# Performance work log

Measured on AMD Instinct MI355X. Metric: run time of the kernel, lower is better.

## Reference

```python
import jax, jax.numpy as jnp
import numpy as np

H = 128          # num_hidden
NIN = 256        # num_in (2*H: edge feat + gathered node feat)
B, L, K = 2, 2048, 48
SCALE = 30.0
LN_EPS = 1e-5


def _layer_norm(x, g, b):
    mu = jnp.mean(x, axis=-1, keepdims=True)
    var = jnp.var(x, axis=-1, keepdims=True)
    return g * (x - mu) * jax.lax.rsqrt(var + LN_EPS) + b


def _gather_nodes(nodes, idx):
    # nodes: [B,L,C], idx: [B,L,K] -> [B,L,K,C]
    return jax.vmap(lambda n, i: n[i])(nodes, idx)


def _gelu(x):
    return jax.nn.gelu(x, approximate=False)  # torch GELU default (erf)


def setup_inputs() -> dict:
    key = jax.random.key(0)
    ks = jax.random.split(key, 24)
    p = lambda k, shp: (jax.random.normal(k, shp, jnp.float32) * 0.05)
    inp = {
        "h_V": jax.random.normal(ks[0], (B, L, H), jnp.float32),
        "h_E": jax.random.normal(ks[1], (B, L, K, H), jnp.float32),
        "E_idx": jax.random.randint(ks[2], (B, L, K), 0, L),
        "mask_V": jnp.ones((B, L), jnp.float32),
        "mask_attend": jnp.ones((B, L, K), jnp.float32),
        # node-message MLP W1-W2-W3
        "W1": p(ks[3], (H + NIN, H)), "b1": jnp.zeros((H,), jnp.float32),
        "W2": p(ks[4], (H, H)), "b2": jnp.zeros((H,), jnp.float32),
        "W3": p(ks[5], (H, H)), "b3": jnp.zeros((H,), jnp.float32),
        # edge-update MLP W11-W12-W13
        "W11": p(ks[6], (H + NIN, H)), "b11": jnp.zeros((H,), jnp.float32),
        "W12": p(ks[7], (H, H)), "b12": jnp.zeros((H,), jnp.float32),
        "W13": p(ks[8], (H, H)), "b13": jnp.zeros((H,), jnp.float32),
        # layer norms
        "g1": jnp.ones((H,), jnp.float32), "be1": jnp.zeros((H,), jnp.float32),
        "g2": jnp.ones((H,), jnp.float32), "be2": jnp.zeros((H,), jnp.float32),
        "g3": jnp.ones((H,), jnp.float32), "be3": jnp.zeros((H,), jnp.float32),
        # position-wise FFN (H -> 4H -> H)
        "W_in": p(ks[9], (H, 4 * H)), "b_in": jnp.zeros((4 * H,), jnp.float32),
        "W_out": p(ks[10], (4 * H, H)), "b_out": jnp.zeros((H,), jnp.float32),
    }
    return inp


def reference(h_V, h_E, E_idx, mask_V, mask_attend,
              W1, b1, W2, b2, W3, b3,
              W11, b11, W12, b12, W13, b13,
              g1, be1, g2, be2, g3, be3,
              W_in, b_in, W_out, b_out):
    # ---- node update: gather neighbors, concat, 3-layer MLP, masked sum ----
    h_nb = _gather_nodes(h_V, E_idx)                       # [B,L,K,H]
    h_EV = jnp.concatenate(
        [jnp.broadcast_to(h_V[:, :, None, :], h_nb.shape), h_E, h_nb], axis=-1)
    h_msg = _gelu(h_EV @ W1 + b1)
    h_msg = _gelu(h_msg @ W2 + b2)
    h_msg = h_msg @ W3 + b3                                # [B,L,K,H]
    h_msg = mask_attend[..., None] * h_msg
    dh = jnp.sum(h_msg, axis=-2) / SCALE                   # [B,L,H]
    h_V = _layer_norm(h_V + dh, g1, be1)
    # ---- position-wise FFN + residual ----
    dh = _gelu(h_V @ W_in + b_in) @ W_out + b_out
    h_V = _layer_norm(h_V + dh, g2, be2)
    h_V = mask_V[..., None] * h_V
    # ---- edge update ----
    h_nb = _gather_nodes(h_V, E_idx)
    h_EV = jnp.concatenate(
        [jnp.broadcast_to(h_V[:, :, None, :], h_nb.shape), h_E, h_nb], axis=-1)
    h_msg = _gelu(h_EV @ W11 + b11)
    h_msg = _gelu(h_msg @ W12 + b12)
    h_msg = h_msg @ W13 + b13
    h_E = _layer_norm(h_E + h_msg, g3, be3)
    return h_V, h_E
```

## Files before the change

### kernel.cpp

```cpp
#include <hip/hip_runtime.h>
#include <hip/hip_bf16.h>
#include <math.h>

#define Hdim 128
#define Kn 48
#define NN 4096
#define FFH 512
#define LN_EPS 1e-5f

typedef __attribute__((ext_vector_type(8))) short bf16x8;
typedef __attribute__((ext_vector_type(4))) float floatx4;
typedef unsigned short ushort_t;

__device__ __forceinline__ float gelu_f(float x) {
    float x2 = x * x;
    float u = x * fmaf(x2, -0.1029454f, -2.3022081f);
    return x * __builtin_amdgcn_rcpf(1.0f + exp2f(u));
}

__device__ __forceinline__ ushort_t f2bf(float f) {
    union { float f; unsigned u; } v;
    v.f = f;
    unsigned r = v.u + 0x7FFF + ((v.u >> 16) & 1);
    return (ushort_t)(r >> 16);
}
__device__ __forceinline__ float bf2f(ushort_t h) {
    union { unsigned u; float f; } v;
    v.u = ((unsigned)h) << 16;
    return v.f;
}

__global__ __launch_bounds__(256) void convert_all(
    const float* __restrict__ W1, const float* __restrict__ W11,
    const float* __restrict__ W2, const float* __restrict__ W3,
    const float* __restrict__ W12, const float* __restrict__ W13,
    const float* __restrict__ W_in, const float* __restrict__ W_out,
    const float* __restrict__ hV, ushort_t* __restrict__ Wt1m,
    ushort_t* __restrict__ Wt11m, ushort_t* __restrict__ Wt2,
    ushort_t* __restrict__ Wt3, ushort_t* __restrict__ Wt12,
    ushort_t* __restrict__ Wt13, ushort_t* __restrict__ WtIn,
    ushort_t* __restrict__ WtOut, ushort_t* __restrict__ hVbf) {
    const int b = blockIdx.x, t = threadIdx.x;
    if (b < 128) {
        int s = b * 256 + t, k = s >> 7, n = s & 127;
        Wt1m[n * 256 + k] = f2bf(W1[16384 + s]);
    } else if (b < 256) {
        int s = (b - 128) * 256 + t, k = s >> 7, n = s & 127;
        Wt11m[n * 256 + k] = f2bf(W11[16384 + s]);
    } else if (b < 320) {
        int s = (b - 256) * 256 + t, k = s >> 7, n = s & 127;
        Wt2[n * 128 + k] = f2bf(W2[s]);
    } else if (b < 384) {
        int s = (b - 320) * 256 + t, k = s >> 7, n = s & 127;
        Wt3[n * 128 + k] = f2bf(W3[s]);
    } else if (b < 448) {
        int s = (b - 384) * 256 + t, k = s >> 7, n = s & 127;
        Wt12[n * 128 + k] = f2bf(W12[s]);
    } else if (b < 512) {
        int s = (b - 448) * 256 + t, k = s >> 7, n = s & 127;
        Wt13[n * 128 + k] = f2bf(W13[s]);
    } else if (b < 768) {
        int s = (b - 512) * 256 + t, k = s >> 9, n = s & 511;
        WtIn[n * 128 + k] = f2bf(W_in[s]);
    } else if (b < 1024) {
        int s = (b - 768) * 256 + t, k = s >> 7, n = s & 127;
        WtOut[n * 512 + k] = f2bf(W_out[s]);
    } else {
        int i = (b - 1024) * 256 + t;
        float4 a = *(const float4*)(hV + (size_t)i * 8);
        float4 c = *(const float4*)(hV + (size_t)i * 8 + 4);
        ushort_t o[8] = {f2bf(a.x), f2bf(a.y), f2bf(a.z), f2bf(a.w),
                         f2bf(c.x), f2bf(c.y), f2bf(c.z), f2bf(c.w)};
        *(uint4*)(hVbf + (size_t)i * 8) = *(const uint4*)o;
    }
}

__global__ __launch_bounds__(128) void pre_self(const float* __restrict__ hV,
                                                const float* __restrict__ W,
                                                const float* __restrict__ b,
                                                float* __restrict__ selfA) {
    __shared__ __align__(16) float xs[8][Hdim];
    const int o = threadIdx.x;
    const int n0 = blockIdx.x * 8;
    for (int n = 0; n < 8; ++n) xs[n][o] = hV[(size_t)(n0 + n) * Hdim + o];
    __syncthreads();
    float acc[8];
    const float bo = b[o];
#pragma unroll
    for (int n = 0; n < 8; ++n) acc[n] = bo;
    for (int i = 0; i < Hdim; i += 4) {
        const float w0 = W[(i + 0) * Hdim + o];
        const float w1 = W[(i + 1) * Hdim + o];
        const float w2 = W[(i + 2) * Hdim + o];
        const float w3 = W[(i + 3) * Hdim + o];
#pragma unroll
        for (int n = 0; n < 8; ++n) {
            const float4 v = *(const float4*)&xs[n][i];
            acc[n] = fmaf(v.x, w0, acc[n]);
            acc[n] = fmaf(v.y, w1, acc[n]);
            acc[n] = fmaf(v.z, w2, acc[n]);
            acc[n] = fmaf(v.w, w3, acc[n]);
        }
    }
#pragma unroll
    for (int n = 0; n < 8; ++n) selfA[(size_t)(n0 + n) * Hdim + o] = acc[n];
}

template <int MODE>
__global__ __launch_bounds__(256, 3) void edge_mlp(
    const float* __restrict__ hV, const float* __restrict__ hE,
    const int* __restrict__ Eidx, const float* __restrict__ maskAtt,
    const float* __restrict__ selfA, const ushort_t* __restrict__ hVbf,
    const ushort_t* __restrict__ WtA, const ushort_t* __restrict__ WtB,
    const ushort_t* __restrict__ WtC, const float* __restrict__ bias2,
    const float* __restrict__ bias3, const float* __restrict__ gamma,
    const float* __restrict__ beta, float* __restrict__ outp) {
    __shared__ __align__(16) char T0[24576];
    __shared__ __align__(16) char T1[12288];
    __shared__ __align__(16) char T2[12288];
    __shared__ int idx_s[Kn];
    __shared__ float dh_s[128];
    __shared__ float rsum[Kn][4], rsum2[Kn][4];
    __shared__ float mu_s[Kn], rs_s[Kn];
    __shared__ float rw[8];

    const int tid = threadIdx.x;
    const int lane = tid & 63;
    const int w = tid >> 6;
    const int l15 = lane & 15, l4 = lane >> 4;
    const int n = blockIdx.x;
    const int n0 = w * 32;
    const int bbase = (n >> 11) << 11;

    if (tid < Kn) idx_s[tid] = Eidx[(size_t)n * Kn + tid];
    {
        const float4* src = (const float4*)(hE + (size_t)n * Kn * Hdim);
#pragma unroll
        for (int it = 0; it < 6; ++it) {
            int i = tid + it * 256;
            float4 v = src[i];
            int row = i >> 5, c = i & 31;
            unsigned lo = f2bf(v.x) | ((unsigned)f2bf(v.y) << 16);
            unsigned hi = f2bf(v.z) | ((unsigned)f2bf(v.w) << 16);
            *(uint2*)(T0 + row * 512 + ((c * 8) ^ ((row & 7) << 4))) =
                make_uint2(lo, hi);
        }
    }
    __syncthreads();
#pragma unroll
    for (int it = 0; it < 3; ++it) {
        int i = tid + it * 256;
        int row = i >> 4, c = i & 15;
        uint4 v =
            *(const uint4*)(hVbf + (size_t)(bbase + idx_s[row]) * Hdim + c * 8);
        *(uint4*)(T0 + row * 512 + ((256 + c * 16) ^ ((row & 7) << 4))) = v;
    }
    __syncthreads();

    floatx4 acc[3][2];
#pragma unroll
    for (int mt = 0; mt < 3; ++mt)
#pragma unroll
        for (int nt = 0; nt < 2; ++nt) acc[mt][nt] = (floatx4)0.0f;

#pragma unroll
    for (int kk = 0; kk < 8; ++kk) {
        bf16x8 a[3], bb[2];
#pragma unroll
        for (int mt = 0; mt < 3; ++mt) {
            int row = mt * 16 + l15;
            a[mt] = *(const bf16x8*)(T0 + row * 512 +
                     ((kk * 64 + l4 * 16) ^ ((row & 7) << 4)));
        }
#pragma unroll
        for (int nt = 0; nt < 2; ++nt)
            bb[nt] = *(const bf16x8*)(WtA + (n0 + nt * 16 + l15) * 256 +
                                      kk * 32 + l4 * 8);
#pragma unroll
        for (int mt = 0; mt < 3; ++mt)
#pragma unroll
            for (int nt = 0; nt < 2; ++nt)
                acc[mt][nt] = __builtin_amdgcn_mfma_f32_16x16x32_bf16(
                    a[mt], bb[nt], acc[mt][nt], 0, 0, 0);
    }
    {
        float sA[2];
#pragma unroll
        for (int nt = 0; nt < 2; ++nt)
            sA[nt] = selfA[(size_t)n * Hdim + n0 + nt * 16 + l15];
#pragma unroll
        for (int mt = 0; mt < 3; ++mt)
#pragma unroll
            for (int nt = 0; nt < 2; ++nt) {
                const int col = n0 + nt * 16 + l15;
#pragma unroll
                for (int r = 0; r < 4; ++r) {
                    float v = gelu_f(acc[mt][nt][r] + sA[nt]);
                    int row = mt * 16 + l4 * 4 + r;
                    *(ushort_t*)(T1 + row * 256 +
                                 ((col * 2) ^ ((row & 7) << 4))) = f2bf(v);
                }
            }
    }
    __syncthreads();

    {
        float bv[2];
#pragma unroll
        for (int nt = 0; nt < 2; ++nt) bv[nt] = bias2[n0 + nt * 16 + l15];
#pragma unroll
        for (int mt = 0; mt < 3; ++mt)
#pragma unroll
            for (int nt = 0; nt < 2; ++nt)
                acc[mt][nt] = (floatx4){bv[nt], bv[nt], bv[nt], bv[nt]};
    }
#pragma unroll
    for (int kk = 0; kk < 4; ++kk) {
        bf16x8 a[3], bb[2];
#pragma unroll
        for (int mt = 0; mt < 3; ++mt) {
            int row = mt * 16 + l15;
            a[mt] = *(const bf16x8*)(T1 + row * 256 +
                     ((kk * 64 + l4 * 16) ^ ((row & 7) << 4)));
        }
#pragma unroll
        for (int nt = 0; nt < 2; ++nt)
            bb[nt] = *(const bf16x8*)(WtB + (n0 + nt * 16 + l15) * 128 +
                                      kk * 32 + l4 * 8);
#pragma unroll
        for (int mt = 0; mt < 3; ++mt)
#pragma unroll
            for (int nt = 0; nt < 2; ++nt)
                acc[mt][nt] = __builtin_amdgcn_mfma_f32_16x16x32_bf16(
                    a[mt], bb[nt], acc[mt][nt], 0, 0, 0);
    }
#pragma unroll
    for (int mt = 0; mt < 3; ++mt)
#pragma unroll
        for (int nt = 0; nt < 2; ++nt) {
            const int col = n0 + nt * 16 + l15;
#pragma unroll
            for (int r = 0; r < 4; ++r) {
                float v = gelu_f(acc[mt][nt][r]);
                int row = mt * 16 + l4 * 4 + r;
                *(ushort_t*)(T2 + row * 256 + ((col * 2) ^ ((row & 7) << 4))) =
                    f2bf(v);
            }
        }
    __syncthreads();

    {
        float bv[2];
#pragma unroll
        for (int nt = 0; nt < 2; ++nt) bv[nt] = bias3[n0 + nt * 16 + l15];
#pragma unroll
        for (int mt = 0; mt < 3; ++mt)
#pragma unroll
            for (int nt = 0; nt < 2; ++nt)
                acc[mt][nt] = (floatx4){bv[nt], bv[nt], bv[nt], bv[nt]};
    }
#pragma unroll
    for (int kk = 0; kk < 4; ++kk) {
        bf16x8 a[3], bb[2];
#pragma unroll
        for (int mt = 0; mt < 3; ++mt) {
            int row = mt * 16 + l15;
            a[mt] = *(const bf16x8*)(T2 + row * 256 +
                     ((kk * 64 + l4 * 16) ^ ((row & 7) << 4)));
        }
#pragma unroll
        for (int nt = 0; nt < 2; ++nt)
            bb[nt] = *(const bf16x8*)(WtC + (n0 + nt * 16 + l15) * 128 +
                                      kk * 32 + l4 * 8);
#pragma unroll
        for (int mt = 0; mt < 3; ++mt)
#pragma unroll
            for (int nt = 0; nt < 2; ++nt)
                acc[mt][nt] = __builtin_amdgcn_mfma_f32_16x16x32_bf16(
                    a[mt], bb[nt], acc[mt][nt], 0, 0, 0);
    }

    if (MODE == 0) {
        float mav[3][4];
#pragma unroll
        for (int mt = 0; mt < 3; ++mt)
#pragma unroll
            for (int r = 0; r < 4; ++r)
                mav[mt][r] =
                    maskAtt[(size_t)n * Kn + mt * 16 + l4 * 4 + r];
#pragma unroll
        for (int nt = 0; nt < 2; ++nt) {
            float c = 0.0f;
#pragma unroll
            for (int mt = 0; mt < 3; ++mt)
#pragma unroll
                for (int r = 0; r < 4; ++r)
                    c = fmaf(mav[mt][r], acc[mt][nt][r], c);
            c += __shfl_xor(c, 16);
            c += __shfl_xor(c, 32);
            if (l4 == 0) dh_s[n0 + nt * 16 + l15] = c;
        }
        __syncthreads();
        float x = 0.0f;
        if (tid < 128) {
            x = hV[(size_t)n * Hdim + tid] + dh_s[tid] * (1.0f / 30.0f);
            float s = x, s2 = x * x;
#pragma unroll
            for (int off = 32; off > 0; off >>= 1) {
                s += __shfl_xor(s, off);
                s2 += __shfl_xor(s2, off);
            }
            if (lane == 0) {
                rw[(tid >> 6) * 2] = s;
                rw[(tid >> 6) * 2 + 1] = s2;
            }
        }
        __syncthreads();
        if (tid < 128) {
            const float ts = rw[0] + rw[2], ts2 = rw[1] + rw[3];
            const float mu = ts * (1.0f / Hdim);
            const float var = ts2 * (1.0f / Hdim) - mu * mu;
            const float rs = rsqrtf(var + LN_EPS);
            outp[(size_t)n * Hdim + tid] =
                gamma[tid] * (x - mu) * rs + beta[tid];
        }
    } else {
        float xv[3][2][4];
#pragma unroll
        for (int mt = 0; mt < 3; ++mt)
#pragma unroll
            for (int nt = 0; nt < 2; ++nt) {
                const int col = n0 + nt * 16 + l15;
#pragma unroll
                for (int r = 0; r < 4; ++r) {
                    int row = mt * 16 + l4 * 4 + r;
                    ushort_t hv = *(const ushort_t*)(
                        T0 + row * 512 + ((col * 2) ^ ((row & 7) << 4)));
                    xv[mt][nt][r] = acc[mt][nt][r] + bf2f(hv);
                }
            }
#pragma unroll
        for (int mt = 0; mt < 3; ++mt)
#pragma unroll
            for (int r = 0; r < 4; ++r) {
                float s = xv[mt][0][r] + xv[mt][1][r];
                float s2 = xv[mt][0][r] * xv[mt][0][r] +
                           xv[mt][1][r] * xv[mt][1][r];
#pragma unroll
                for (int off = 1; off < 16; off <<= 1) {
                    s += __shfl_xor(s, off);
                    s2 += __shfl_xor(s2, off);
                }
                if (l15 == 0) {
                    int row = mt * 16 + l4 * 4 + r;
                    rsum[row][w] = s;
                    rsum2[row][w] = s2;
                }
            }
        __syncthreads();
        if (tid < Kn) {
            float s = rsum[tid][0] + rsum[tid][1] + rsum[tid][2] + rsum[tid][3];
            float s2 =
                rsum2[tid][0] + rsum2[tid][1] + rsum2[tid][2] + rsum2[tid][3];
            float mu = s * (1.0f / Hdim);
            float var = s2 * (1.0f / Hdim) - mu * mu;
            mu_s[tid] = mu;
            rs_s[tid] = rsqrtf(var + LN_EPS);
        }
        __syncthreads();
        float gv[2], bv[2];
#pragma unroll
        for (int nt = 0; nt < 2; ++nt) {
            gv[nt] = gamma[n0 + nt * 16 + l15];
            bv[nt] = beta[n0 + nt * 16 + l15];
        }
#pragma unroll
        for (int mt = 0; mt < 3; ++mt)
#pragma unroll
            for (int nt = 0; nt < 2; ++nt) {
                const int col = n0 + nt * 16 + l15;
#pragma unroll
                for (int r = 0; r < 4; ++r) {
                    int row = mt * 16 + l4 * 4 + r;
                    float y = gv[nt] * (xv[mt][nt][r] - mu_s[row]) *
                                  rs_s[row] + bv[nt];
                    outp[((size_t)n * Kn + row) * Hdim + col] = y;
                }
            }
    }
}

__global__ __launch_bounds__(512) void ffn_mfma(
    const float* __restrict__ hV2, const ushort_t* __restrict__ WtIn,
    const float* __restrict__ b_in, const ushort_t* __restrict__ WtOut,
    const float* __restrict__ b_out, const float* __restrict__ g2,
    const float* __restrict__ be2, const float* __restrict__ maskV,
    float* __restrict__ outp, ushort_t* __restrict__ outb) {
    __shared__ __align__(16) char XF[8192];
    __shared__ __align__(16) char HF[32768];
    __shared__ float rsF[32][4], rs2F[32][4], muF[32], rstdF[32];

    const int tid = threadIdx.x;
    const int lane = tid & 63;
    const int w = tid >> 6;
    const int wm = w >> 2, wc = w & 3;
    const int l15 = lane & 15, l4 = lane >> 4;
    const int rg0 = blockIdx.x * 32;

    {
        const float4* src = (const float4*)(hV2 + (size_t)rg0 * Hdim);
#pragma unroll
        for (int it = 0; it < 2; ++it) {
            int i = tid + it * 512;
            float4 v = src[i];
            int row = i >> 5, c = i & 31;
            unsigned lo = f2bf(v.x) | ((unsigned)f2bf(v.y) << 16);
            unsigned hi = f2bf(v.z) | ((unsigned)f2bf(v.w) << 16);
            *(uint2*)(XF + row * 256 + ((c * 8) ^ ((row & 7) << 4))) =
                make_uint2(lo, hi);
        }
    }
    __syncthreads();
    {
        floatx4 a1[8];
#pragma unroll
        for (int j = 0; j < 8; ++j) {
            float bv = b_in[wc * 128 + j * 16 + l15];
            a1[j] = (floatx4){bv, bv, bv, bv};
        }
#pragma unroll
        for (int kk = 0; kk < 4; ++kk) {
            int row = wm * 16 + l15;
            bf16x8 af = *(const bf16x8*)(XF + row * 256 +
                         ((kk * 64 + l4 * 16) ^ ((row & 7) << 4)));
#pragma unroll
            for (int j = 0; j < 8; ++j) {
                bf16x8 bf = *(const bf16x8*)(WtIn +
                             (wc * 128 + j * 16 + l15) * 128 + kk * 32 +
                             l4 * 8);
                a1[j] = __builtin_amdgcn_mfma_f32_16x16x32_bf16(af, bf, a1[j],
                                                                0, 0, 0);
            }
        }
#pragma unroll
        for (int j = 0; j < 8; ++j) {
            const int col = wc * 128 + j * 16 + l15;
#pragma unroll
            for (int r = 0; r < 4; ++r) {
                int row = wm * 16 + l4 * 4 + r;
                float v = gelu_f(a1[j][r]);
                *(ushort_t*)(HF + row * 1024 +
                             ((col * 2) ^ ((row & 7) << 4))) = f2bf(v);
            }
        }
    }
    __syncthreads();
    floatx4 o2[2];
#pragma unroll
    for (int nt = 0; nt < 2; ++nt) {
        float bv = b_out[(wc * 2 + nt) * 16 + l15];
        o2[nt] = (floatx4){bv, bv, bv, bv};
    }
#pragma unroll
    for (int kk = 0; kk < 16; ++kk) {
        int row = wm * 16 + l15;
        bf16x8 af = *(const bf16x8*)(HF + row * 1024 +
                     ((kk * 64 + l4 * 16) ^ ((row & 7) << 4)));
#pragma unroll
        for (int nt = 0; nt < 2; ++nt) {
            bf16x8 bf = *(const bf16x8*)(WtOut +
                         ((wc * 2 + nt) * 16 + l15) * 512 + kk * 32 + l4 * 8);
            o2[nt] = __builtin_amdgcn_mfma_f32_16x16x32_bf16(af, bf, o2[nt],
                                                             0, 0, 0);
        }
    }
    float xv[2][4];
#pragma unroll
    for (int nt = 0; nt < 2; ++nt) {
        const int col = (wc * 2 + nt) * 16 + l15;
#pragma unroll
        for (int r = 0; r < 4; ++r) {
            int row = wm * 16 + l4 * 4 + r;
            xv[nt][r] = hV2[(size_t)(rg0 + row) * Hdim + col] + o2[nt][r];
        }
    }
#pragma unroll
    for (int r = 0; r < 4; ++r) {
        float s = xv[0][r] + xv[1][r];
        float s2 = xv[0][r] * xv[0][r] + xv[1][r] * xv[1][r];
#pragma unroll
        for (int off = 1; off < 16; off <<= 1) {
            s += __shfl_xor(s, off);
            s2 += __shfl_xor(s2, off);
        }
        if (l15 == 0) {
            int row = wm * 16 + l4 * 4 + r;
            rsF[row][wc] = s;
            rs2F[row][wc] = s2;
        }
    }
    __syncthreads();
    if (tid < 32) {
        float s = rsF[tid][0] + rsF[tid][1] + rsF[tid][2] + rsF[tid][3];
        float s2 = rs2F[tid][0] + rs2F[tid][1] + rs2F[tid][2] + rs2F[tid][3];
        float mu = s * (1.0f / Hdim);
        float var = s2 * (1.0f / Hdim) - mu * mu;
        muF[tid] = mu;
        rstdF[tid] = rsqrtf(var + LN_EPS);
    }
    __syncthreads();
#pragma unroll
    for (int nt = 0; nt < 2; ++nt) {
        const int col = (wc * 2 + nt) * 16 + l15;
        float gvv = g2[col], bvv = be2[col];
#pragma unroll
        for (int r = 0; r < 4; ++r) {
            int row = wm * 16 + l4 * 4 + r;
            float y = (gvv * (xv[nt][r] - muF[row]) * rstdF[row] + bvv) *
                      maskV[rg0 + row];
            outp[(size_t)(rg0 + row) * Hdim + col] = y;
            outb[(size_t)(rg0 + row) * Hdim + col] = f2bf(y);
        }
    }
}

extern "C" void kernel_launch(void* const* d_in, const int* in_sizes, int n_in,
                              void* d_out, int out_size, void* d_ws,
                              size_t ws_size, hipStream_t stream) {
    const float* hV = (const float*)d_in[0];
    const float* hE = (const float*)d_in[1];
    const int* Eidx = (const int*)d_in[2];
    const float* maskV = (const float*)d_in[3];
    const float* maskAtt = (const float*)d_in[4];
    const float* W1 = (const float*)d_in[5];
    const float* b1 = (const float*)d_in[6];
    const float* W2 = (const float*)d_in[7];
    const float* b2 = (const float*)d_in[8];
    const float* W3 = (const float*)d_in[9];
    const float* b3 = (const float*)d_in[10];
    const float* W11 = (const float*)d_in[11];
    const float* b11 = (const float*)d_in[12];
    const float* W12 = (const float*)d_in[13];
    const float* b12 = (const float*)d_in[14];
    const float* W13 = (const float*)d_in[15];
    const float* b13 = (const float*)d_in[16];
    const float* g1 = (const float*)d_in[17];
    const float* be1 = (const float*)d_in[18];
    const float* g2 = (const float*)d_in[19];
    const float* be2 = (const float*)d_in[20];
    const float* g3 = (const float*)d_in[21];
    const float* be3 = (const float*)d_in[22];
    const float* W_in = (const float*)d_in[23];
    const float* b_in = (const float*)d_in[24];
    const float* W_out = (const float*)d_in[25];
    const float* b_out = (const float*)d_in[26];

    float* out_hV = (float*)d_out;
    float* out_hE = out_hV + (size_t)NN * Hdim;
    float* ws = (float*)d_ws;
    float* hV2 = ws;
    float* selfA = ws + 524288;
    ushort_t* u = (ushort_t*)(ws + 1048576);
    ushort_t* hVbf = u;
    ushort_t* outVbf = u + 524288;
    ushort_t* Wt1m = u + 1048576;
    ushort_t* Wt11m = u + 1081344;
    ushort_t* Wt2 = u + 1114112;
    ushort_t* Wt3 = u + 1130496;
    ushort_t* Wt12 = u + 1146880;
    ushort_t* Wt13 = u + 1163264;
    ushort_t* WtIn = u + 1179648;
    ushort_t* WtOut = u + 1245184;

    convert_all<<<1280, 256, 0, stream>>>(W1, W11, W2, W3, W12, W13, W_in,
                                          W_out, hV, Wt1m, Wt11m, Wt2, Wt3,
                                          Wt12, Wt13, WtIn, WtOut, hVbf);
    pre_self<<<NN / 8, 128, 0, stream>>>(hV, W1, b1, selfA);
    edge_mlp<0><<<NN, 256, 0, stream>>>(hV, hE, Eidx, maskAtt, selfA, hVbf,
                                        Wt1m, Wt2, Wt3, b2, b3, g1, be1, hV2);
    ffn_mfma<<<NN / 32, 512, 0, stream>>>(hV2, WtIn, b_in, WtOut, b_out, g2,
                                          be2, maskV, out_hV, outVbf);
    pre_self<<<NN / 8, 128, 0, stream>>>(out_hV, W11, b11, selfA);
    edge_mlp<1><<<NN, 256, 0, stream>>>(nullptr, hE, Eidx, nullptr, selfA,
                                        outVbf, Wt11m, Wt12, Wt13, b12, b13,
                                        g3, be3, out_hE);
}
```

Baseline: 411.5 us.

## Fuse self-projection into convert and FFN kernels, pre-tile weights for MFMA

Removes the two standalone pre_self launches. The first self-projection moves into convert_all, and the second into the FFN kernel, which now does a bf16 MFMA against a new W11 self-part weight. Weights are pre-packed into an MFMA fragment-tiled layout through a shared-memory transpose. Edge and FFN shared tiles switch to a column-major padded layout. T2 now aliases T0, which cuts shared memory so edge_mlp can request 4 blocks per SM, at the cost of an extra barrier. The FFN is retiled to 16 rows per block, and the second self-projection now runs in bf16, which slightly changes precision.

```diff
diff --git a/kernel.cpp b/kernel.cpp
--- a/kernel.cpp
+++ b/kernel.cpp
@@ -12,6 +12,8 @@
 typedef __attribute__((ext_vector_type(4))) float floatx4;
 typedef unsigned short ushort_t;
 
+#define CMA(row, col) ((((col) >> 3) * 784) + ((row) << 4) + (((col)&7) << 1))
+
 __device__ __forceinline__ float gelu_f(float x) {
     float x2 = x * x;
     float u = x * fmaf(x2, -0.1029454f, -2.3022081f);
@@ -19,10 +21,8 @@
 }
 
 __device__ __forceinline__ ushort_t f2bf(float f) {
-    union { float f; unsigned u; } v;
-    v.f = f;
-    unsigned r = v.u + 0x7FFF + ((v.u >> 16) & 1);
-    return (ushort_t)(r >> 16);
+    __hip_bfloat16 h = __float2bfloat16(f);
+    return *reinterpret_cast<ushort_t*>(&h);
 }
 __device__ __forceinline__ float bf2f(ushort_t h) {
     union { unsigned u; float f; } v;
@@ -35,79 +35,91 @@
     const float* __restrict__ W2, const float* __restrict__ W3,
     const float* __restrict__ W12, const float* __restrict__ W13,
     const float* __restrict__ W_in, const float* __restrict__ W_out,
-    const float* __restrict__ hV, ushort_t* __restrict__ Wt1m,
-    ushort_t* __restrict__ Wt11m, ushort_t* __restrict__ Wt2,
+    const float* __restrict__ hV, const float* __restrict__ b1,
+    ushort_t* __restrict__ Wt1m, ushort_t* __restrict__ Wt11m,
+    ushort_t* __restrict__ Wt11a, ushort_t* __restrict__ Wt2,
     ushort_t* __restrict__ Wt3, ushort_t* __restrict__ Wt12,
     ushort_t* __restrict__ Wt13, ushort_t* __restrict__ WtIn,
-    ushort_t* __restrict__ WtOut, ushort_t* __restrict__ hVbf) {
+    ushort_t* __restrict__ WtOut, ushort_t* __restrict__ hVbf,
+    float* __restrict__ selfA) {
+    __shared__ __align__(16) char cmem[8448];
     const int b = blockIdx.x, t = threadIdx.x;
-    if (b < 128) {
-        int s = b * 256 + t, k = s >> 7, n = s & 127;
-        Wt1m[n * 256 + k] = f2bf(W1[16384 + s]);
-    } else if (b < 256) {
-        int s = (b - 128) * 256 + t, k = s >> 7, n = s & 127;
-        Wt11m[n * 256 + k] = f2bf(W11[16384 + s]);
-    } else if (b < 320) {
-        int s = (b - 256) * 256 + t, k = s >> 7, n = s & 127;
-        Wt2[n * 128 + k] = f2bf(W2[s]);
-    } else if (b < 384) {
-        int s = (b - 320) * 256 + t, k = s >> 7, n = s & 127;
-        Wt3[n * 128 + k] = f2bf(W3[s]);
-    } else if (b < 448) {
-        int s = (b - 384) * 256 + t, k = s >> 7, n = s & 127;
-        Wt12[n * 128 + k] = f2bf(W12[s]);
-    } else if (b < 512) {
-        int s = (b - 448) * 256 + t, k = s >> 7, n = s & 127;
-        Wt13[n * 128 + k] = f2bf(W13[s]);
-    } else if (b < 768) {
-        int s = (b - 512) * 256 + t, k = s >> 9, n = s & 511;
-        WtIn[n * 128 + k] = f2bf(W_in[s]);
-    } else if (b < 1024) {
-        int s = (b - 768) * 256 + t, k = s >> 7, n = s & 127;
-        WtOut[n * 512 + k] = f2bf(W_out[s]);
-    } else {
-        int i = (b - 1024) * 256 + t;
-        float4 a = *(const float4*)(hV + (size_t)i * 8);
-        float4 c = *(const float4*)(hV + (size_t)i * 8 + 4);
+
+    if (b < 272) {
+        const float* src;
+        ushort_t* dst;
+        int K, C, rowOff, tile;
+        if (b < 32)       { src = W1;   dst = Wt1m;  K = 256; C = 128; rowOff = 128; tile = b; }
+        else if (b < 64)  { src = W11;  dst = Wt11m; K = 256; C = 128; rowOff = 128; tile = b - 32; }
+        else if (b < 80)  { src = W11;  dst = Wt11a; K = 128; C = 128; rowOff = 0;   tile = b - 64; }
+        else if (b < 96)  { src = W2;   dst = Wt2;   K = 128; C = 128; rowOff = 0;   tile = b - 80; }
+        else if (b < 112) { src = W3;   dst = Wt3;   K = 128; C = 128; rowOff = 0;   tile = b - 96; }
+        else if (b < 128) { src = W12;  dst = Wt12;  K = 128; C = 128; rowOff = 0;   tile = b - 112; }
+        else if (b < 144) { src = W13;  dst = Wt13;  K = 128; C = 128; rowOff = 0;   tile = b - 128; }
+        else if (b < 208) { src = W_in; dst = WtIn;  K = 128; C = 512; rowOff = 0;   tile = b - 144; }
+        else              { src = W_out;dst = WtOut; K = 512; C = 128; rowOff = 0;   tile = b - 208; }
+        const int tpr = C >> 5;
+        const int tk = tile / tpr, tn = tile % tpr;
+        const int tr0 = tk * 32, tc0 = tn * 32;
+        const int KD32 = K >> 5;
+        float (*s)[33] = (float(*)[33])cmem;
+#pragma unroll
+        for (int i = 0; i < 4; ++i) {
+            int r = (t >> 5) + i * 8, c = t & 31;
+            s[r][c] = src[(size_t)(rowOff + tr0 + r) * C + tc0 + c];
+        }
+        __syncthreads();
+        if (t < 128) {
+            int n_loc = t >> 2, kc0 = (t & 3) * 8;
+            int n = tc0 + n_loc, k = tr0 + kc0;
+            ushort_t o[8];
+#pragma unroll
+            for (int e = 0; e < 8; ++e) o[e] = f2bf(s[kc0 + e][n_loc]);
+            size_t idx = (size_t)((n >> 4) * KD32 + (k >> 5)) * 512 +
+                         ((k >> 3) & 3) * 128 + (n & 15) * 8;
+            *(uint4*)(dst + idx) = *(const uint4*)o;
+        }
+    } else if (b < 528) {
+        int i = (b - 272) * 2048 + t * 8;
+        float4 a = *(const float4*)(hV + (size_t)i);
+        float4 c = *(const float4*)(hV + (size_t)i + 4);
         ushort_t o[8] = {f2bf(a.x), f2bf(a.y), f2bf(a.z), f2bf(a.w),
                          f2bf(c.x), f2bf(c.y), f2bf(c.z), f2bf(c.w)};
-        *(uint4*)(hVbf + (size_t)i * 8) = *(const uint4*)o;
-    }
-}
-
-__global__ __launch_bounds__(128) void pre_self(const float* __restrict__ hV,
-                                                const float* __restrict__ W,
-                                                const float* __restrict__ b,
-                                                float* __restrict__ selfA) {
-    __shared__ __align__(16) float xs[8][Hdim];
-    const int o = threadIdx.x;
-    const int n0 = blockIdx.x * 8;
-    for (int n = 0; n < 8; ++n) xs[n][o] = hV[(size_t)(n0 + n) * Hdim + o];
-    __syncthreads();
-    float acc[8];
-    const float bo = b[o];
-#pragma unroll
-    for (int n = 0; n < 8; ++n) acc[n] = bo;
-    for (int i = 0; i < Hdim; i += 4) {
-        const float w0 = W[(i + 0) * Hdim + o];
-        const float w1 = W[(i + 1) * Hdim + o];
-        const float w2 = W[(i + 2) * Hdim + o];
-        const float w3 = W[(i + 3) * Hdim + o];
-#pragma unroll
-        for (int n = 0; n < 8; ++n) {
-            const float4 v = *(const float4*)&xs[n][i];
-            acc[n] = fmaf(v.x, w0, acc[n]);
-            acc[n] = fmaf(v.y, w1, acc[n]);
-            acc[n] = fmaf(v.z, w2, acc[n]);
-            acc[n] = fmaf(v.w, w3, acc[n]);
-        }
-    }
-#pragma unroll
-    for (int n = 0; n < 8; ++n) selfA[(size_t)(n0 + n) * Hdim + o] = acc[n];
+        *(uint4*)(hVbf + (size_t)i) = *(const uint4*)o;
+    } else {
+        float (*xs)[Hdim] = (float(*)[Hdim])cmem;
+        const int grp = t >> 7, o = t & 127;
+        const int nb0 = (b - 528) * 16;
+#pragma unroll
+        for (int n = 0; n < 8; ++n)
+            xs[grp * 8 + n][o] = hV[(size_t)(nb0 + grp * 8 + n) * Hdim + o];
+        __syncthreads();
+        float acc[8];
+        const float bo = b1[o];
+#pragma unroll
+        for (int n = 0; n < 8; ++n) acc[n] = bo;
+        for (int i = 0; i < Hdim; i += 4) {
+            const float w0 = W1[(i + 0) * Hdim + o];
+            const float w1 = W1[(i + 1) * Hdim + o];
+            const float w2 = W1[(i + 2) * Hdim + o];
+            const float w3 = W1[(i + 3) * Hdim + o];
+#pragma unroll
+            for (int n = 0; n < 8; ++n) {
+                const float4 v = *(const float4*)&xs[grp * 8 + n][i];
+                acc[n] = fmaf(v.x, w0, acc[n]);
+                acc[n] = fmaf(v.y, w1, acc[n]);
+                acc[n] = fmaf(v.z, w2, acc[n]);
+                acc[n] = fmaf(v.w, w3, acc[n]);
+            }
+        }
+#pragma unroll
+        for (int n = 0; n < 8; ++n)
+            selfA[(size_t)(nb0 + grp * 8 + n) * Hdim + o] = acc[n];
+    }
 }
 
 template <int MODE>
-__global__ __launch_bounds__(256, 3) void edge_mlp(
+__global__ __launch_bounds__(256, 4) void edge_mlp(
     const float* __restrict__ hV, const float* __restrict__ hE,
     const int* __restrict__ Eidx, const float* __restrict__ maskAtt,
     const float* __restrict__ selfA, const ushort_t* __restrict__ hVbf,
@@ -115,14 +127,14 @@
     const ushort_t* __restrict__ WtC, const float* __restrict__ bias2,
     const float* __restrict__ bias3, const float* __restrict__ gamma,
     const float* __restrict__ beta, float* __restrict__ outp) {
-    __shared__ __align__(16) char T0[24576];
-    __shared__ __align__(16) char T1[12288];
-    __shared__ __align__(16) char T2[12288];
+    __shared__ __align__(16) char T0[32 * 784];
+    __shared__ __align__(16) char T1[16 * 784];
     __shared__ int idx_s[Kn];
     __shared__ float dh_s[128];
     __shared__ float rsum[Kn][4], rsum2[Kn][4];
     __shared__ float mu_s[Kn], rs_s[Kn];
     __shared__ float rw[8];
+    char* T2 = T0 + 16 * 784;
 
     const int tid = threadIdx.x;
     const int lane = tid & 63;
@@ -131,6 +143,8 @@
     const int n = blockIdx.x;
     const int n0 = w * 32;
     const int bbase = (n >> 11) << 11;
+    const int abase = l4 * 784 + l15 * 16;
+    const int fbase = l4 * 128 + l15 * 8;
 
     if (tid < Kn) idx_s[tid] = Eidx[(size_t)n * Kn + tid];
     {
@@ -139,10 +153,10 @@
         for (int it = 0; it < 6; ++it) {
             int i = tid + it * 256;
             float4 v = src[i];
-            int row = i >> 5, c = i & 31;
+            int row = i >> 5, j = i & 31;
             unsigned lo = f2bf(v.x) | ((unsigned)f2bf(v.y) << 16);
             unsigned hi = f2bf(v.z) | ((unsigned)f2bf(v.w) << 16);
-            *(uint2*)(T0 + row * 512 + ((c * 8) ^ ((row & 7) << 4))) =
+            *(uint2*)(T0 + (j >> 1) * 784 + row * 16 + (j & 1) * 8) =
                 make_uint2(lo, hi);
         }
     }
@@ -153,7 +167,7 @@
         int row = i >> 4, c = i & 15;
         uint4 v =
             *(const uint4*)(hVbf + (size_t)(bbase + idx_s[row]) * Hdim + c * 8);
-        *(uint4*)(T0 + row * 512 + ((256 + c * 16) ^ ((row & 7) << 4))) = v;
+        *(uint4*)(T0 + (16 + c) * 784 + row * 16) = v;
     }
     __syncthreads();
 
@@ -167,15 +181,12 @@
     for (int kk = 0; kk < 8; ++kk) {
         bf16x8 a[3], bb[2];
 #pragma unroll
-        for (int mt = 0; mt < 3; ++mt) {
-            int row = mt * 16 + l15;
-            a[mt] = *(const bf16x8*)(T0 + row * 512 +
-                     ((kk * 64 + l4 * 16) ^ ((row & 7) << 4)));
-        }
+        for (int mt = 0; mt < 3; ++mt)
+            a[mt] = *(const bf16x8*)(T0 + abase + mt * 256 + kk * 3136);
 #pragma unroll
         for (int nt = 0; nt < 2; ++nt)
-            bb[nt] = *(const bf16x8*)(WtA + (n0 + nt * 16 + l15) * 256 +
-                                      kk * 32 + l4 * 8);
+            bb[nt] = *(const bf16x8*)(WtA + ((w * 2 + nt) * 8 + kk) * 512 +
+                                      fbase);
 #pragma unroll
         for (int mt = 0; mt < 3; ++mt)
 #pragma unroll
@@ -197,8 +208,7 @@
                 for (int r = 0; r < 4; ++r) {
                     float v = gelu_f(acc[mt][nt][r] + sA[nt]);
                     int row = mt * 16 + l4 * 4 + r;
-                    *(ushort_t*)(T1 + row * 256 +
-                                 ((col * 2) ^ ((row & 7) << 4))) = f2bf(v);
+                    *(ushort_t*)(T1 + CMA(row, col)) = f2bf(v);
                 }
             }
     }
@@ -218,15 +228,12 @@
     for (int kk = 0; kk < 4; ++kk) {
         bf16x8 a[3], bb[2];
 #pragma unroll
-        for (int mt = 0; mt < 3; ++mt) {
-            int row = mt * 16 + l15;
-            a[mt] = *(const bf16x8*)(T1 + row * 256 +
-                     ((kk * 64 + l4 * 16) ^ ((row & 7) << 4)));
-        }
+        for (int mt = 0; mt < 3; ++mt)
+            a[mt] = *(const bf16x8*)(T1 + abase + mt * 256 + kk * 3136);
 #pragma unroll
         for (int nt = 0; nt < 2; ++nt)
-            bb[nt] = *(const bf16x8*)(WtB + (n0 + nt * 16 + l15) * 128 +
-                                      kk * 32 + l4 * 8);
+            bb[nt] = *(const bf16x8*)(WtB + ((w * 2 + nt) * 4 + kk) * 512 +
+                                      fbase);
 #pragma unroll
         for (int mt = 0; mt < 3; ++mt)
 #pragma unroll
@@ -234,6 +241,7 @@
                 acc[mt][nt] = __builtin_amdgcn_mfma_f32_16x16x32_bf16(
                     a[mt], bb[nt], acc[mt][nt], 0, 0, 0);
     }
+    __syncthreads();
 #pragma unroll
     for (int mt = 0; mt < 3; ++mt)
 #pragma unroll
@@ -243,8 +251,7 @@
             for (int r = 0; r < 4; ++r) {
                 float v = gelu_f(acc[mt][nt][r]);
                 int row = mt * 16 + l4 * 4 + r;
-                *(ushort_t*)(T2 + row * 256 + ((col * 2) ^ ((row & 7) << 4))) =
-                    f2bf(v);
+                *(ushort_t*)(T2 + CMA(row, col)) = f2bf(v);
             }
         }
     __syncthreads();
@@ -263,15 +270,12 @@
     for (int kk = 0; kk < 4; ++kk) {
         bf16x8 a[3], bb[2];
 #pragma unroll
-        for (int mt = 0; mt < 3; ++mt) {
-            int row = mt * 16 + l15;
-            a[mt] = *(const bf16x8*)(T2 + row * 256 +
-                     ((kk * 64 + l4 * 16) ^ ((row & 7) << 4)));
-        }
+        for (int mt = 0; mt < 3; ++mt)
+            a[mt] = *(const bf16x8*)(T2 + abase + mt * 256 + kk * 3136);
 #pragma unroll
         for (int nt = 0; nt < 2; ++nt)
-            bb[nt] = *(const bf16x8*)(WtC + (n0 + nt * 16 + l15) * 128 +
-                                      kk * 32 + l4 * 8);
+            bb[nt] = *(const bf16x8*)(WtC + ((w * 2 + nt) * 4 + kk) * 512 +
+                                      fbase);
 #pragma unroll
         for (int mt = 0; mt < 3; ++mt)
 #pragma unroll
@@ -286,8 +290,7 @@
         for (int mt = 0; mt < 3; ++mt)
 #pragma unroll
             for (int r = 0; r < 4; ++r)
-                mav[mt][r] =
-                    maskAtt[(size_t)n * Kn + mt * 16 + l4 * 4 + r];
+                mav[mt][r] = maskAtt[(size_t)n * Kn + mt * 16 + l4 * 4 + r];
 #pragma unroll
         for (int nt = 0; nt < 2; ++nt) {
             float c = 0.0f;
@@ -311,8 +314,8 @@
                 s2 += __shfl_xor(s2, off);
             }
             if (lane == 0) {
-                rw[(tid >> 6) * 2] = s;
-                rw[(tid >> 6) * 2 + 1] = s2;
+                rw[w * 2] = s;
+                rw[w * 2 + 1] = s2;
             }
         }
         __syncthreads();
@@ -334,8 +337,7 @@
 #pragma unroll
                 for (int r = 0; r < 4; ++r) {
                     int row = mt * 16 + l4 * 4 + r;
-                    ushort_t hv = *(const ushort_t*)(
-                        T0 + row * 512 + ((col * 2) ^ ((row & 7) << 4)));
+                    ushort_t hv = *(const ushort_t*)(T0 + CMA(row, col));
                     xv[mt][nt][r] = acc[mt][nt][r] + bf2f(hv);
                 }
             }
@@ -393,134 +395,131 @@
 __global__ __launch_bounds__(512) void ffn_mfma(
     const float* __restrict__ hV2, const ushort_t* __restrict__ WtIn,
     const float* __restrict__ b_in, const ushort_t* __restrict__ WtOut,
-    const float* __restrict__ b_out, const float* __restrict__ g2,
+    const float* __restrict__ b_out, const ushort_t* __restrict__ Wt11a,
+    const float* __restrict__ b11, const float* __restrict__ g2,
     const float* __restrict__ be2, const float* __restrict__ maskV,
-    float* __restrict__ outp, ushort_t* __restrict__ outb) {
-    __shared__ __align__(16) char XF[8192];
-    __shared__ __align__(16) char HF[32768];
-    __shared__ float rsF[32][4], rs2F[32][4], muF[32], rstdF[32];
+    float* __restrict__ outp, ushort_t* __restrict__ outb,
+    float* __restrict__ selfA2) {
+    __shared__ __align__(16) char XF[16 * 272];
+    __shared__ __align__(16) char HF[64 * 272];
+    __shared__ float rsF[16][8], rs2F[16][8], muF[16], rstdF[16];
 
     const int tid = threadIdx.x;
     const int lane = tid & 63;
     const int w = tid >> 6;
-    const int wm = w >> 2, wc = w & 3;
     const int l15 = lane & 15, l4 = lane >> 4;
-    const int rg0 = blockIdx.x * 32;
+    const int rg0 = blockIdx.x * 16;
+    const int abase = l4 * 272 + l15 * 16;
+    const int fbase = l4 * 128 + l15 * 8;
 
     {
         const float4* src = (const float4*)(hV2 + (size_t)rg0 * Hdim);
-#pragma unroll
-        for (int it = 0; it < 2; ++it) {
-            int i = tid + it * 512;
-            float4 v = src[i];
-            int row = i >> 5, c = i & 31;
-            unsigned lo = f2bf(v.x) | ((unsigned)f2bf(v.y) << 16);
-            unsigned hi = f2bf(v.z) | ((unsigned)f2bf(v.w) << 16);
-            *(uint2*)(XF + row * 256 + ((c * 8) ^ ((row & 7) << 4))) =
-                make_uint2(lo, hi);
-        }
-    }
-    __syncthreads();
-    {
-        floatx4 a1[8];
-#pragma unroll
-        for (int j = 0; j < 8; ++j) {
-            float bv = b_in[wc * 128 + j * 16 + l15];
+        int i = tid;
+        float4 v = src[i];
+        int row = i >> 5, j = i & 31;
+        unsigned lo = f2bf(v.x) | ((unsigned)f2bf(v.y) << 16);
+        unsigned hi = f2bf(v.z) | ((unsigned)f2bf(v.w) << 16);
+        *(uint2*)(XF + (j >> 1) * 272 + row * 16 + (j & 1) * 8) =
+            make_uint2(lo, hi);
+    }
+    __syncthreads();
+    {
+        floatx4 a1[4];
+#pragma unroll
+        for (int j = 0; j < 4; ++j) {
+            float bv = b_in[(w * 4 + j) * 16 + l15];
             a1[j] = (floatx4){bv, bv, bv, bv};
         }
 #pragma unroll
         for (int kk = 0; kk < 4; ++kk) {
-            int row = wm * 16 + l15;
-            bf16x8 af = *(const bf16x8*)(XF + row * 256 +
-                         ((kk * 64 + l4 * 16) ^ ((row & 7) << 4)));
-#pragma unroll
-            for (int j = 0; j < 8; ++j) {
+            bf16x8 af = *(const bf16x8*)(XF + abase + kk * 1088);
+#pragma unroll
+            for (int j = 0; j < 4; ++j) {
                 bf16x8 bf = *(const bf16x8*)(WtIn +
-                             (wc * 128 + j * 16 + l15) * 128 + kk * 32 +
-                             l4 * 8);
+                             ((w * 4 + j) * 4 + kk) * 512 + fbase);
                 a1[j] = __builtin_amdgcn_mfma_f32_16x16x32_bf16(af, bf, a1[j],
                                                                 0, 0, 0);
             }
         }
 #pragma unroll
-        for (int j = 0; j < 8; ++j) {
-            const int col = wc * 128 + j * 16 + l15;
+        for (int j = 0; j < 4; ++j) {
+            const int col = (w * 4 + j) * 16 + l15;
 #pragma unroll
             for (int r = 0; r < 4; ++r) {
-                int row = wm * 16 + l4 * 4 + r;
-                float v = gelu_f(a1[j][r]);
-                *(ushort_t*)(HF + row * 1024 +
-                             ((col * 2) ^ ((row & 7) << 4))) = f2bf(v);
-            }
-        }
-    }
-    __syncthreads();
-    floatx4 o2[2];
-#pragma unroll
-    for (int nt = 0; nt < 2; ++nt) {
-        float bv = b_out[(wc * 2 + nt) * 16 + l15];
-        o2[nt] = (floatx4){bv, bv, bv, bv};
+                int row = l4 * 4 + r;
+                *(ushort_t*)(HF + ((col >> 3) * 272) + row * 16 +
+                             ((col & 7) << 1)) = f2bf(gelu_f(a1[j][r]));
+            }
+        }
+    }
+    __syncthreads();
+    floatx4 o2;
+    {
+        float bv = b_out[w * 16 + l15];
+        o2 = (floatx4){bv, bv, bv, bv};
     }
 #pragma unroll
     for (int kk = 0; kk < 16; ++kk) {
-        int row = wm * 16 + l15;
-        bf16x8 af = *(const bf16x8*)(HF + row * 1024 +
-                     ((kk * 64 + l4 * 16) ^ ((row & 7) << 4)));
-#pragma unroll
-        for (int nt = 0; nt < 2; ++nt) {
-            bf16x8 bf = *(const bf16x8*)(WtOut +
-                         ((wc * 2 + nt) * 16 + l15) * 512 + kk * 32 + l4 * 8);
-            o2[nt] = __builtin_amdgcn_mfma_f32_16x16x32_bf16(af, bf, o2[nt],
-                                                             0, 0, 0);
-        }
-    }
-    float xv[2][4];
-#pragma unroll
-    for (int nt = 0; nt < 2; ++nt) {
-        const int col = (wc * 2 + nt) * 16 + l15;
-#pragma unroll
-        for (int r = 0; r < 4; ++r) {
-            int row = wm * 16 + l4 * 4 + r;
-            xv[nt][r] = hV2[(size_t)(rg0 + row) * Hdim + col] + o2[nt][r];
-        }
-    }
+        bf16x8 af = *(const bf16x8*)(HF + abase + kk * 1088);
+        bf16x8 bf = *(const bf16x8*)(WtOut + (w * 16 + kk) * 512 + fbase);
+        o2 = __builtin_amdgcn_mfma_f32_16x16x32_bf16(af, bf, o2, 0, 0, 0);
+    }
+    const int colw = w * 16 + l15;
+    float xv[4];
+#pragma unroll
+    for (int r = 0; r < 4; ++r)
+        xv[r] = hV2[(size_t)(rg0 + l4 * 4 + r) * Hdim + colw] + o2[r];
 #pragma unroll
     for (int r = 0; r < 4; ++r) {
-        float s = xv[0][r] + xv[1][r];
-        float s2 = xv[0][r] * xv[0][r] + xv[1][r] * xv[1][r];
+        float s = xv[r], s2 = xv[r] * xv[r];
 #pragma unroll
         for (int off = 1; off < 16; off <<= 1) {
             s += __shfl_xor(s, off);
             s2 += __shfl_xor(s2, off);
         }
         if (l15 == 0) {
-            int row = wm * 16 + l4 * 4 + r;
-            rsF[row][wc] = s;
-            rs2F[row][wc] = s2;
-        }
-    }
-    __syncthreads();
-    if (tid < 32) {
-        float s = rsF[tid][0] + rsF[tid][1] + rsF[tid][2] + rsF[tid][3];
-        float s2 = rs2F[tid][0] + rs2F[tid][1] + rs2F[tid][2] + rs2F[tid][3];
+            rsF[l4 * 4 + r][w] = s;
+            rs2F[l4 * 4 + r][w] = s2;
+        }
+    }
+    __syncthreads();
+    if (tid < 16) {
+        float s = 0.0f, s2 = 0.0f;
+#pragma unroll
+        for (int q = 0; q < 8; ++q) { s += rsF[tid][q]; s2 += rs2F[tid][q]; }
         float mu = s * (1.0f / Hdim);
         float var = s2 * (1.0f / Hdim) - mu * mu;
         muF[tid] = mu;
         rstdF[tid] = rsqrtf(var + LN_EPS);
     }
     __syncthreads();
-#pragma unroll
-    for (int nt = 0; nt < 2; ++nt) {
-        const int col = (wc * 2 + nt) * 16 + l15;
-        float gvv = g2[col], bvv = be2[col];
+    {
+        float gvv = g2[colw], bvv = be2[colw];
 #pragma unroll
         for (int r = 0; r < 4; ++r) {
-            int row = wm * 16 + l4 * 4 + r;
-            float y = (gvv * (xv[nt][r] - muF[row]) * rstdF[row] + bvv) *
+            int row = l4 * 4 + r;
+            float y = (gvv * (xv[r] - muF[row]) * rstdF[row] + bvv) *
                       maskV[rg0 + row];
-            outp[(size_t)(rg0 + row) * Hdim + col] = y;
-            outb[(size_t)(rg0 + row) * Hdim + col] = f2bf(y);
-        }
+            ushort_t yb = f2bf(y);
+            outp[(size_t)(rg0 + row) * Hdim + colw] = y;
+            outb[(size_t)(rg0 + row) * Hdim + colw] = yb;
+            *(ushort_t*)(XF + ((colw >> 3) * 272) + row * 16 +
+                         ((colw & 7) << 1)) = yb;
+        }
+    }
+    __syncthreads();
+    {
+        float bv = b11[colw];
+        floatx4 sa = (floatx4){bv, bv, bv, bv};
+#pragma unroll
+        for (int kk = 0; kk < 4; ++kk) {
+            bf16x8 af = *(const bf16x8*)(XF + abase + kk * 1088);
+            bf16x8 bf = *(const bf16x8*)(Wt11a + (w * 4 + kk) * 512 + fbase);
+            sa = __builtin_amdgcn_mfma_f32_16x16x32_bf16(af, bf, sa, 0, 0, 0);
+        }
+#pragma unroll
+        for (int r = 0; r < 4; ++r)
+            selfA2[(size_t)(rg0 + l4 * 4 + r) * Hdim + colw] = sa[r];
     }
 }
 
@@ -565,22 +564,23 @@
     ushort_t* outVbf = u + 524288;
     ushort_t* Wt1m = u + 1048576;
     ushort_t* Wt11m = u + 1081344;
-    ushort_t* Wt2 = u + 1114112;
-    ushort_t* Wt3 = u + 1130496;
-    ushort_t* Wt12 = u + 1146880;
-    ushort_t* Wt13 = u + 1163264;
-    ushort_t* WtIn = u + 1179648;
-    ushort_t* WtOut = u + 1245184;
-
-    convert_all<<<1280, 256, 0, stream>>>(W1, W11, W2, W3, W12, W13, W_in,
-                                          W_out, hV, Wt1m, Wt11m, Wt2, Wt3,
-                                          Wt12, Wt13, WtIn, WtOut, hVbf);
-    pre_self<<<NN / 8, 128, 0, stream>>>(hV, W1, b1, selfA);
+    ushort_t* Wt11a = u + 1114112;
+    ushort_t* Wt2 = u + 1130496;
+    ushort_t* Wt3 = u + 1146880;
+    ushort_t* Wt12 = u + 1163264;
+    ushort_t* Wt13 = u + 1179648;
+    ushort_t* WtIn = u + 1196032;
+    ushort_t* WtOut = u + 1261568;
+
+    convert_all<<<784, 256, 0, stream>>>(W1, W11, W2, W3, W12, W13, W_in,
+                                         W_out, hV, b1, Wt1m, Wt11m, Wt11a,
+                                         Wt2, Wt3, Wt12, Wt13, WtIn, WtOut,
+                                         hVbf, selfA);
     edge_mlp<0><<<NN, 256, 0, stream>>>(hV, hE, Eidx, maskAtt, selfA, hVbf,
                                         Wt1m, Wt2, Wt3, b2, b3, g1, be1, hV2);
-    ffn_mfma<<<NN / 32, 512, 0, stream>>>(hV2, WtIn, b_in, WtOut, b_out, g2,
-                                          be2, maskV, out_hV, outVbf);
-    pre_self<<<NN / 8, 128, 0, stream>>>(out_hV, W11, b11, selfA);
+    ffn_mfma<<<NN / 16, 512, 0, stream>>>(hV2, WtIn, b_in, WtOut, b_out,
+                                          Wt11a, b11, g2, be2, maskV, out_hV,
+                                          outVbf, selfA);
     edge_mlp<1><<<NN, 256, 0, stream>>>(nullptr, hE, Eidx, nullptr, selfA,
                                         outVbf, Wt11m, Wt12, Wt13, b12, b13,
                                         g3, be3, out_hE);
```

New measurement: 330.0 us. 1.25x faster.
